# Performance work log

Measured on AMD Instinct MI355X. Metric: run time of the kernel, lower is better.

## Reference

```python
import jax, jax.numpy as jnp
import numpy as np

NNODE = 500000       # nodes -> 2*NNODE global DOFs
NELEM = 500000       # elements, 8 DOF each (2D quad)
NDOF = 2 * NNODE


def setup_inputs() -> dict:
    key = jax.random.key(0)
    k1, k2, k3, k4 = jax.random.split(key, 4)
    u = jax.random.normal(k1, (NDOF,), dtype=jnp.float32)
    weight1 = jax.random.normal(k2, (NDOF,), dtype=jnp.float32)
    bc_idx = jnp.arange(NDOF, dtype=jnp.int64)  # free-DOF indices (all free)
    # elemental DOF map: 8 global DOF indices per element (irregular)
    edof = jax.random.randint(k3, (NELEM, 8), 0, NDOF, dtype=jnp.int64)
    # per-element 8x8 stiffness matrices
    stiffness = jax.random.normal(k4, (NELEM, 8, 8), dtype=jnp.float32)
    return {"u": u, "weight1": weight1, "bc_idx": bc_idx,
            "edof": edof, "stiffness": stiffness}


def reference(u, weight1, bc_idx, edof, stiffness):
    # u1 = zeros; u1[bc_idx] = weight1 * u[bc_idx]
    u1 = jnp.zeros_like(u).at[bc_idx].set(weight1 * u[bc_idx])
    # gather elemental DOF values: [E, 8]
    ue = u1[edof]
    # per-element stiffness matvec: [E, 8]
    fe = jnp.einsum('eij,ej->ei', stiffness, ue)
    # scatter-add assembly into global force vector
    F = jnp.zeros_like(u).at[edof.reshape(-1)].add(fe.reshape(-1))
    return F
```

## Files before the change

### kernel.cpp

```cpp
#include <hip/hip_runtime.h>

typedef float          vfloat4  __attribute__((ext_vector_type(4)));
typedef int            vint4    __attribute__((ext_vector_type(4)));
typedef unsigned int   vuint4   __attribute__((ext_vector_type(4)));

#define BSHIFT 12
#define BSIZE  4096
#define NBMAX  256
#define TPBC   512
#define CAP    32
#define OCAP   128
#define CAPB   20480
#define TPB    256

__global__ void scatter_u1_kernel(const float* __restrict__ u,
                                  const float* __restrict__ w1,
                                  const int* __restrict__ bc,
                                  float* __restrict__ u1, int n,
                                  int* __restrict__ gpos) {
    if (blockIdx.x == 0 && threadIdx.x < NBMAX) gpos[threadIdx.x] = 0;
    int k = blockIdx.x * blockDim.x + threadIdx.x;
    if (k < n) {
        int idx = bc[k];
        u1[idx] = w1[k] * u[idx];
    }
}

__global__ __launch_bounds__(TPBC, 4)
void compute_scatter_kernel(const float* __restrict__ u1,
                            const int* __restrict__ edof,
                            const float* __restrict__ stiff,
                            int* __restrict__ gpos,
                            unsigned int* __restrict__ pairs,
                            int nelem, int nb) {
    __shared__ unsigned int lstage[NBMAX * CAP];
    __shared__ int c[NBMAX];
    __shared__ int gb[NBMAX];
    __shared__ int spos[NBMAX + 1];
    __shared__ unsigned long long oflow[OCAP];
    __shared__ int noflow;

    int tid = threadIdx.x;
    int e   = blockIdx.x * TPBC + tid;
    if (tid < NBMAX) c[tid] = 0;
    if (tid == 0) noflow = 0;
    __syncthreads();

    if (e < nelem) {
        const vint4* ep = (const vint4*)(edof + (size_t)e * 8);
        vint4 ia = __builtin_nontemporal_load(ep);
        vint4 ib = __builtin_nontemporal_load(ep + 1);
        int idx[8] = {ia.x, ia.y, ia.z, ia.w, ib.x, ib.y, ib.z, ib.w};

        float ue[8];
        #pragma unroll
        for (int j = 0; j < 8; ++j) ue[j] = u1[idx[j]];

        const vfloat4* Kp = (const vfloat4*)(stiff + (size_t)e * 64);
        unsigned int ent[8];
        #pragma unroll
        for (int i = 0; i < 8; ++i) {
            vfloat4 ka = __builtin_nontemporal_load(Kp + 2 * i);
            vfloat4 kb = __builtin_nontemporal_load(Kp + 2 * i + 1);
            float fe;
            fe  = ka.x * ue[0] + ka.y * ue[1] + ka.z * ue[2] + ka.w * ue[3];
            fe += kb.x * ue[4] + kb.y * ue[5] + kb.z * ue[6] + kb.w * ue[7];
            unsigned short hu = __builtin_bit_cast(unsigned short, (_Float16)fe);
            ent[i] = ((unsigned)(idx[i] & (BSIZE - 1)) << 16) | (unsigned)hu;
        }
        #pragma unroll
        for (int i = 0; i < 8; ++i) {
            int b  = idx[i] >> BSHIFT;
            int rk = atomicAdd(&c[b], 1);
            if (rk < CAP) {
                lstage[b * CAP + rk] = ent[i];
            } else {
                int o = atomicAdd(&noflow, 1);
                if (o < OCAP)
                    oflow[o] = ((unsigned long long)(((unsigned)b << 16) | (unsigned)rk) << 32)
                             | (unsigned long long)ent[i];
            }
        }
    }
    __syncthreads();

    if (tid < nb) gb[tid] = atomicAdd(&gpos[tid], c[tid]);
    if (tid < 64) {
        int v[4];
        int s = 0;
        for (int j = 0; j < 4; ++j) {
            int b = tid * 4 + j;
            v[j] = (b < nb) ? min(c[b], CAP) : 0;
            s += v[j];
        }
        int incl = s;
        for (int off = 1; off < 64; off <<= 1) {
            int n = __shfl_up(incl, off, 64);
            if (tid >= off) incl += n;
        }
        int run = incl - s;
        for (int j = 0; j < 4; ++j) { spos[tid * 4 + j] = run; run += v[j]; }
        if (tid == 63) spos[NBMAX] = incl;
    }
    __syncthreads();

    int S = spos[nb];
    for (int t = tid; t < S; t += TPBC) {
        int lo = 0, hi = nb;
        while (hi - lo > 1) {
            int mid = (lo + hi) >> 1;
            if (spos[mid] <= t) lo = mid; else hi = mid;
        }
        int r = t - spos[lo];
        pairs[(size_t)lo * CAPB + gb[lo] + r] = lstage[lo * CAP + r];
    }
    int no = min(noflow, OCAP);
    for (int t = tid; t < no; t += TPBC) {
        unsigned long long w2 = oflow[t];
        unsigned int en = (unsigned int)w2;
        unsigned int hi2 = (unsigned int)(w2 >> 32);
        int b = (int)(hi2 >> 16);
        int r = (int)(hi2 & 0xffffu);
        pairs[(size_t)b * CAPB + gb[b] + r] = en;
    }
}

__global__ void bucket_reduce_kernel(const unsigned int* __restrict__ pairs,
                                     const int* __restrict__ gpos,
                                     float* __restrict__ F, int ndof) {
    __shared__ float acc[BSIZE];
    int b = blockIdx.x;
    for (int j = threadIdx.x; j < BSIZE; j += 1024) acc[j] = 0.0f;
    __syncthreads();
    int len = gpos[b];
    size_t base = (size_t)b * CAPB;
    int len4 = len & ~3;
    for (int k = threadIdx.x * 4; k < len4; k += 1024 * 4) {
        vuint4 p = __builtin_nontemporal_load((const vuint4*)(pairs + base + k));
        atomicAdd(&acc[p.x >> 16], (float)__builtin_bit_cast(_Float16, (unsigned short)(p.x & 0xffffu)));
        atomicAdd(&acc[p.y >> 16], (float)__builtin_bit_cast(_Float16, (unsigned short)(p.y & 0xffffu)));
        atomicAdd(&acc[p.z >> 16], (float)__builtin_bit_cast(_Float16, (unsigned short)(p.z & 0xffffu)));
        atomicAdd(&acc[p.w >> 16], (float)__builtin_bit_cast(_Float16, (unsigned short)(p.w & 0xffffu)));
    }
    for (int k = len4 + threadIdx.x; k < len; k += 1024) {
        unsigned p = pairs[base + k];
        atomicAdd(&acc[p >> 16], (float)__builtin_bit_cast(_Float16, (unsigned short)(p & 0xffffu)));
    }
    __syncthreads();
    int gbase = b << BSHIFT;
    for (int j = threadIdx.x; j < BSIZE; j += 1024) {
        int g = gbase + j;
        if (g < ndof) F[g] = acc[j];
    }
}

__global__ void elem_assemble_kernel(const float* __restrict__ u1,
                                     const int* __restrict__ edof,
                                     const float* __restrict__ stiff,
                                     float* __restrict__ F, int nelem) {
    int t = blockIdx.x * blockDim.x + threadIdx.x;
    int e = t >> 3;
    if (e >= nelem) return;
    int i = t & 7;
    int idx = __builtin_nontemporal_load(edof + t);
    float ue = u1[idx];
    const vfloat4* Kr = (const vfloat4*)(stiff + (size_t)e * 64 + (size_t)i * 8);
    vfloat4 k0 = __builtin_nontemporal_load(Kr);
    vfloat4 k1 = __builtin_nontemporal_load(Kr + 1);
    float fe;
    fe  = k0.x * __shfl(ue, 0, 8);
    fe += k0.y * __shfl(ue, 1, 8);
    fe += k0.z * __shfl(ue, 2, 8);
    fe += k0.w * __shfl(ue, 3, 8);
    fe += k1.x * __shfl(ue, 4, 8);
    fe += k1.y * __shfl(ue, 5, 8);
    fe += k1.z * __shfl(ue, 6, 8);
    fe += k1.w * __shfl(ue, 7, 8);
    unsafeAtomicAdd(&F[idx], fe);
}

extern "C" void kernel_launch(void* const* d_in, const int* in_sizes, int n_in,
                              void* d_out, int out_size, void* d_ws, size_t ws_size,
                              hipStream_t stream) {
    const float* u     = (const float*)d_in[0];
    const float* w1    = (const float*)d_in[1];
    const int*   bc    = (const int*)d_in[2];
    const int*   edof  = (const int*)d_in[3];
    const float* stiff = (const float*)d_in[4];
    float* F = (float*)d_out;

    int ndof  = in_sizes[0];
    int nbc   = in_sizes[2];
    int total = in_sizes[3];
    int nelem = total / 8;
    int nb    = (ndof + BSIZE - 1) >> BSHIFT;

    char* w = (char*)d_ws;
    size_t o = 0;
    auto take = [&](size_t nbytes) -> char* {
        char* p = w + o;
        o += (nbytes + 255) & ~(size_t)255;
        return p;
    };
    float* u1 = (float*)take((size_t)ndof * 4);
    unsigned int* pairs = (unsigned int*)take((size_t)nb * CAPB * 4);
    int* gpos = (int*)take((size_t)NBMAX * 4);

    (void)hipMemsetAsync(u1, 0, (size_t)ndof * sizeof(float), stream);
    scatter_u1_kernel<<<(nbc + TPB - 1) / TPB, TPB, 0, stream>>>(u, w1, bc, u1, nbc, gpos);

    if (o <= ws_size && nb <= NBMAX && total % 8 == 0) {
        int grid = (nelem + TPBC - 1) / TPBC;
        compute_scatter_kernel<<<grid, TPBC, 0, stream>>>(
            u1, edof, stiff, gpos, pairs, nelem, nb);
        bucket_reduce_kernel<<<nb, 1024, 0, stream>>>(pairs, gpos, F, ndof);
    } else {
        (void)hipMemsetAsync(F, 0, (size_t)ndof * sizeof(float), stream);
        elem_assemble_kernel<<<(total + TPB - 1) / TPB, TPB, 0, stream>>>(
            u1, edof, stiff, F, nelem);
    }
}
```

Measured before the change: 308.1 us.

## Map one thread per stiffness row with shuffles and batch rows per thread

The compute-and-bin kernel now gives each thread one matrix row instead of a whole element. Each thread handles 8 strided rows across the block's 4096-entry batch, and the 8 element DOF values are shared among 8 lanes with shuffles. This makes edof and stiffness reads coalesced across lanes and cuts per-thread register use. Launch bounds are raised to 8 blocks per CU, and the per-bucket LDS staging capacity is cut from 32 to 28 (overflow buffer raised to 192) so LDS fits that occupancy. The smaller staging capacity raises the risk of overflow entries beyond the buffer being silently dropped.

```diff
diff --git a/kernel.cpp b/kernel.cpp
--- a/kernel.cpp
+++ b/kernel.cpp
@@ -8,8 +8,10 @@
 #define BSIZE  4096
 #define NBMAX  256
 #define TPBC   512
-#define CAP    32
-#define OCAP   128
+#define RPT    8
+#define BATCH  (TPBC * RPT)
+#define CAP    28
+#define OCAP   192
 #define CAPB   20480
 #define TPB    256
 
@@ -26,13 +28,13 @@
     }
 }
 
-__global__ __launch_bounds__(TPBC, 4)
+__global__ __launch_bounds__(TPBC, 8)
 void compute_scatter_kernel(const float* __restrict__ u1,
                             const int* __restrict__ edof,
                             const float* __restrict__ stiff,
                             int* __restrict__ gpos,
                             unsigned int* __restrict__ pairs,
-                            int nelem, int nb) {
+                            int total, int nb) {
     __shared__ unsigned int lstage[NBMAX * CAP];
     __shared__ int c[NBMAX];
     __shared__ int gb[NBMAX];
@@ -41,44 +43,53 @@
     __shared__ int noflow;
 
     int tid = threadIdx.x;
-    int e   = blockIdx.x * TPBC + tid;
+    int k0  = blockIdx.x * BATCH;
     if (tid < NBMAX) c[tid] = 0;
     if (tid == 0) noflow = 0;
     __syncthreads();
 
-    if (e < nelem) {
-        const vint4* ep = (const vint4*)(edof + (size_t)e * 8);
-        vint4 ia = __builtin_nontemporal_load(ep);
-        vint4 ib = __builtin_nontemporal_load(ep + 1);
-        int idx[8] = {ia.x, ia.y, ia.z, ia.w, ib.x, ib.y, ib.z, ib.w};
-
-        float ue[8];
-        #pragma unroll
-        for (int j = 0; j < 8; ++j) ue[j] = u1[idx[j]];
-
-        const vfloat4* Kp = (const vfloat4*)(stiff + (size_t)e * 64);
-        unsigned int ent[8];
-        #pragma unroll
-        for (int i = 0; i < 8; ++i) {
-            vfloat4 ka = __builtin_nontemporal_load(Kp + 2 * i);
-            vfloat4 kb = __builtin_nontemporal_load(Kp + 2 * i + 1);
+    int   idxs[RPT];
+    float ues[RPT];
+    #pragma unroll
+    for (int r = 0; r < RPT; ++r) {
+        int k = k0 + r * TPBC + tid;
+        idxs[r] = (k < total) ? __builtin_nontemporal_load(edof + k) : 0;
+    }
+    #pragma unroll
+    for (int r = 0; r < RPT; ++r) ues[r] = u1[idxs[r]];
+
+    #pragma unroll
+    for (int r = 0; r < RPT; ++r) {
+        int k = k0 + r * TPBC + tid;
+        if (k < total) {
+            int e = k >> 3;
+            int i = k & 7;
+            const vfloat4* Kr = (const vfloat4*)(stiff + (size_t)e * 64 + (size_t)i * 8);
+            vfloat4 ka = __builtin_nontemporal_load(Kr);
+            vfloat4 kb = __builtin_nontemporal_load(Kr + 1);
+            float ue = ues[r];
             float fe;
-            fe  = ka.x * ue[0] + ka.y * ue[1] + ka.z * ue[2] + ka.w * ue[3];
-            fe += kb.x * ue[4] + kb.y * ue[5] + kb.z * ue[6] + kb.w * ue[7];
+            fe  = ka.x * __shfl(ue, 0, 8);
+            fe += ka.y * __shfl(ue, 1, 8);
+            fe += ka.z * __shfl(ue, 2, 8);
+            fe += ka.w * __shfl(ue, 3, 8);
+            fe += kb.x * __shfl(ue, 4, 8);
+            fe += kb.y * __shfl(ue, 5, 8);
+            fe += kb.z * __shfl(ue, 6, 8);
+            fe += kb.w * __shfl(ue, 7, 8);
+
             unsigned short hu = __builtin_bit_cast(unsigned short, (_Float16)fe);
-            ent[i] = ((unsigned)(idx[i] & (BSIZE - 1)) << 16) | (unsigned)hu;
-        }
-        #pragma unroll
-        for (int i = 0; i < 8; ++i) {
-            int b  = idx[i] >> BSHIFT;
+            int idx = idxs[r];
+            unsigned int ent = ((unsigned)(idx & (BSIZE - 1)) << 16) | (unsigned)hu;
+            int b  = idx >> BSHIFT;
             int rk = atomicAdd(&c[b], 1);
             if (rk < CAP) {
-                lstage[b * CAP + rk] = ent[i];
+                lstage[b * CAP + rk] = ent;
             } else {
                 int o = atomicAdd(&noflow, 1);
                 if (o < OCAP)
                     oflow[o] = ((unsigned long long)(((unsigned)b << 16) | (unsigned)rk) << 32)
-                             | (unsigned long long)ent[i];
+                             | (unsigned long long)ent;
             }
         }
     }
@@ -117,7 +128,7 @@
     int no = min(noflow, OCAP);
     for (int t = tid; t < no; t += TPBC) {
         unsigned long long w2 = oflow[t];
-        unsigned int en = (unsigned int)w2;
+        unsigned int en  = (unsigned int)w2;
         unsigned int hi2 = (unsigned int)(w2 >> 32);
         int b = (int)(hi2 >> 16);
         int r = (int)(hi2 & 0xffffu);
@@ -210,9 +221,9 @@
     scatter_u1_kernel<<<(nbc + TPB - 1) / TPB, TPB, 0, stream>>>(u, w1, bc, u1, nbc, gpos);
 
     if (o <= ws_size && nb <= NBMAX && total % 8 == 0) {
-        int grid = (nelem + TPBC - 1) / TPBC;
+        int grid = (total + BATCH - 1) / BATCH;
         compute_scatter_kernel<<<grid, TPBC, 0, stream>>>(
-            u1, edof, stiff, gpos, pairs, nelem, nb);
+            u1, edof, stiff, gpos, pairs, total, nb);
         bucket_reduce_kernel<<<nb, 1024, 0, stream>>>(pairs, gpos, F, ndof);
     } else {
         (void)hipMemsetAsync(F, 0, (size_t)ndof * sizeof(float), stream);
```

Result: faster. 260.7 us (-15.4%).
